# Performance work log

Hardware: AMD Instinct MI355X
Metric: run time of the kernel (lower is better)

The kernel has to match this reference:

```python
import jax, jax.numpy as jnp
import numpy as np

N_II = 100000      # item nodes
N_UIU = 200000     # user + item nodes
D = 64             # embedding_dim
E_II = 600000
E_UIU = 1200000
L_II = 3           # num_layers_ii
L_UIU = 3          # num_layers_uiu
N_USERS = 100000   # items occupy indices [N_USERS, N_USERS+N_II)


def _lightgcn_embedding(x, edge_index, edge_weight, num_layers, num_nodes):
    """PyG LightGCN.get_embedding: symmetric gcn_norm (no self loops) + mean over layer outputs."""
    src, dst = edge_index[0], edge_index[1]
    # gcn_norm: deg over target nodes, weighted by edge_weight
    deg = jax.ops.segment_sum(edge_weight, dst, num_segments=num_nodes)
    deg_inv_sqrt = jnp.where(deg > 0, jax.lax.rsqrt(jnp.where(deg > 0, deg, 1.0)), 0.0)
    norm = deg_inv_sqrt[src] * edge_weight * deg_inv_sqrt[dst]  # [E]
    alpha = 1.0 / (num_layers + 1)
    out = x * alpha
    for _ in range(num_layers):
        # SpMM: gather source embeddings, scale, scatter-add to targets
        x = jax.ops.segment_sum(norm[:, None] * x[src], dst, num_segments=num_nodes)  # [N, D]
        out = out + x * alpha
    return out


def setup_inputs() -> dict:
    key = jax.random.key(0)
    k1, k2, k3, k4, k5, k6 = jax.random.split(key, 6)
    return {
        "emb_ii": jax.random.normal(k1, (N_II, D), dtype=jnp.float32),
        "emb_uiu": jax.random.normal(k2, (N_UIU, D), dtype=jnp.float32),
        "edge_attr_ii": jax.random.uniform(k3, (E_II,), dtype=jnp.float32),
        "edge_attr_uiu": jax.random.uniform(k4, (E_UIU,), dtype=jnp.float32),
        "edge_index_ii": jax.random.randint(k5, (2, E_II), 0, N_II, dtype=jnp.int32),
        "edge_index_uiu": jax.random.randint(k6, (2, E_UIU), 0, N_UIU, dtype=jnp.int32),
        # contiguous item block starting at N_USERS (node_mask_item.nonzero())
        "item_idx": jnp.arange(N_II, dtype=jnp.int32) + N_USERS,
    }


def reference(emb_ii, emb_uiu, edge_attr_ii, edge_attr_uiu,
              edge_index_ii, edge_index_uiu, item_idx):
    # item-item graph propagation
    h_ii = _lightgcn_embedding(emb_ii, edge_index_ii, edge_attr_ii, L_II, N_II)  # [N_II, D]
    # write item embeddings into the user-item embedding table
    emb_uiu = emb_uiu.at[item_idx].set(h_ii)
    # user-item graph propagation
    h_uiu = _lightgcn_embedding(emb_uiu, edge_index_uiu, edge_attr_uiu, L_UIU, N_UIU)  # [N_UIU, D]
    return h_uiu
```

## Files before the change

### kernel.cpp

```cpp
#include <hip/hip_runtime.h>


#define D       64
#define N_II    100000
#define N_UIU   200000
#define E_II    600000
#define E_UIU   1200000
#define N_USERS 100000

__device__ __forceinline__ unsigned short f2bf(float f) {
    unsigned u = __float_as_uint(f);
    u += 0x7fffu + ((u >> 16) & 1u);
    return (unsigned short)(u >> 16);
}
__device__ __forceinline__ void bf8_fma(float acc[8], uint4 p, float v) {
    acc[0] += v * __uint_as_float(p.x << 16);
    acc[1] += v * __uint_as_float(p.x & 0xffff0000u);
    acc[2] += v * __uint_as_float(p.y << 16);
    acc[3] += v * __uint_as_float(p.y & 0xffff0000u);
    acc[4] += v * __uint_as_float(p.z << 16);
    acc[5] += v * __uint_as_float(p.z & 0xffff0000u);
    acc[6] += v * __uint_as_float(p.w << 16);
    acc[7] += v * __uint_as_float(p.w & 0xffff0000u);
}
__device__ __forceinline__ void bf8_add(float acc[8], uint4 p) {
    acc[0] += __uint_as_float(p.x << 16);
    acc[1] += __uint_as_float(p.x & 0xffff0000u);
    acc[2] += __uint_as_float(p.y << 16);
    acc[3] += __uint_as_float(p.y & 0xffff0000u);
    acc[4] += __uint_as_float(p.z << 16);
    acc[5] += __uint_as_float(p.z & 0xffff0000u);
    acc[6] += __uint_as_float(p.w << 16);
    acc[7] += __uint_as_float(p.w & 0xffff0000u);
}
__device__ __forceinline__ uint4 pack8(const float a[8]) {
    uint4 r;
    r.x = (unsigned)f2bf(a[0]) | ((unsigned)f2bf(a[1]) << 16);
    r.y = (unsigned)f2bf(a[2]) | ((unsigned)f2bf(a[3]) << 16);
    r.z = (unsigned)f2bf(a[4]) | ((unsigned)f2bf(a[5]) << 16);
    r.w = (unsigned)f2bf(a[6]) | ((unsigned)f2bf(a[7]) << 16);
    return r;
}


__global__ void k_cnt_rank(const int* __restrict__ dst, int* __restrict__ cnt,
                           int* __restrict__ rank, int E) {
    int e = blockIdx.x * blockDim.x + threadIdx.x;
    if (e < E) rank[e] = atomicAdd(&cnt[dst[e]], 1);
}

__global__ void k_rowoff(const int* __restrict__ cnt, int* __restrict__ roff,
                         int* __restrict__ rend, int* __restrict__ gcur, int N) {
    __shared__ int sh[256];
    __shared__ int base;
    int t = threadIdx.x;
    int i = blockIdx.x * 256 + t;
    int v = (i < N) ? cnt[i] : 0;
    sh[t] = v;
    __syncthreads();
    for (int off = 1; off < 256; off <<= 1) {
        int u = (t >= off) ? sh[t - off] : 0;
        __syncthreads();
        sh[t] += u;
        __syncthreads();
    }
    if (t == 255) base = atomicAdd(gcur, sh[255]);
    __syncthreads();
    if (i < N) {
        int o = base + sh[t] - v;
        roff[i] = o;
        rend[i] = o + v;
    }
}

__global__ void k_fillE(const int* __restrict__ src, const int* __restrict__ dst,
                        const float* __restrict__ w, const int* __restrict__ rank,
                        const int* __restrict__ roff, int2* __restrict__ ev, int E) {
    int e = blockIdx.x * blockDim.x + threadIdx.x;
    if (e < E) {
        int pos = roff[dst[e]] + rank[e];
        ev[pos] = make_int2(src[e], __float_as_int(w[e]));
    }
}

__global__ void k_deg_dis(const int* __restrict__ roff, const int* __restrict__ rend,
                          const int2* __restrict__ ev, float* __restrict__ dis, int N) {
    int i = blockIdx.x * blockDim.x + threadIdx.x;
    if (i >= N) return;
    float dg = 0.f;
    for (int j = roff[i]; j < rend[i]; ++j) dg += __int_as_float(ev[j].y);
    dis[i] = (dg > 0.f) ? rsqrtf(dg) : 0.f;
}

__global__ void k_val(const int* __restrict__ roff, const int* __restrict__ rend,
                      const float* __restrict__ dis, int2* __restrict__ ev, int N) {
    int i = blockIdx.x * blockDim.x + threadIdx.x;
    if (i >= N) return;
    float di = dis[i];
    for (int j = roff[i]; j < rend[i]; ++j) {
        int2 p = ev[j];
        ev[j].y = __float_as_int(di * __int_as_float(p.y) * dis[p.x]);
    }
}

__global__ void k_cvt(const float4* __restrict__ x, uint4* __restrict__ xb, int n8) {
    int i = blockIdx.x * blockDim.x + threadIdx.x;
    if (i >= n8) return;
    float4 a = x[2 * i], b = x[2 * i + 1];
    float t[8] = {a.x, a.y, a.z, a.w, b.x, b.y, b.z, b.w};
    xb[i] = pack8(t);
}

__global__ void k_spmm8(const int* __restrict__ roff, const int* __restrict__ rend,
                        const int2* __restrict__ ev, const uint4* __restrict__ xb,
                        uint4* __restrict__ xn, int N) {
    int idx = blockIdx.x * blockDim.x + threadIdx.x;
    int row = idx >> 3;
    if (row >= N) return;
    int g = idx & 7;
    int s = roff[row], e = rend[row];
    float acc[8] = {0.f, 0.f, 0.f, 0.f, 0.f, 0.f, 0.f, 0.f};
    int j = s;
    for (; j + 1 < e; j += 2) {
        int2 p0 = ev[j], p1 = ev[j + 1];
        uint4 a0 = xb[p0.x * 8 + g];
        uint4 a1 = xb[p1.x * 8 + g];
        bf8_fma(acc, a0, __int_as_float(p0.y));
        bf8_fma(acc, a1, __int_as_float(p1.y));
    }
    if (j < e) {
        int2 p0 = ev[j];
        uint4 a0 = xb[p0.x * 8 + g];
        bf8_fma(acc, a0, __int_as_float(p0.y));
    }
    xn[row * 8 + g] = pack8(acc);
}

__global__ void k_spmm8_final(const int* __restrict__ roff, const int* __restrict__ rend,
                              const int2* __restrict__ ev, const uint4* __restrict__ x2b,
                              const uint4* __restrict__ x1b, const float4* __restrict__ x0,
                              float4* __restrict__ out, uint4* __restrict__ outb,
                              float alpha, int N) {
    int idx = blockIdx.x * blockDim.x + threadIdx.x;
    int row = idx >> 3;
    if (row >= N) return;
    int g = idx & 7;
    int s = roff[row], e = rend[row];
    float acc[8] = {0.f, 0.f, 0.f, 0.f, 0.f, 0.f, 0.f, 0.f};
    int j = s;
    for (; j + 1 < e; j += 2) {
        int2 p0 = ev[j], p1 = ev[j + 1];
        uint4 a0 = x2b[p0.x * 8 + g];
        uint4 a1 = x2b[p1.x * 8 + g];
        bf8_fma(acc, a0, __int_as_float(p0.y));
        bf8_fma(acc, a1, __int_as_float(p1.y));
    }
    if (j < e) {
        int2 p0 = ev[j];
        uint4 a0 = x2b[p0.x * 8 + g];
        bf8_fma(acc, a0, __int_as_float(p0.y));
    }
    bf8_add(acc, x1b[row * 8 + g]);
    bf8_add(acc, x2b[row * 8 + g]);
    float4 b0 = x0[row * 16 + 2 * g];
    float4 b1 = x0[row * 16 + 2 * g + 1];
    float r[8] = {alpha * (b0.x + acc[0]), alpha * (b0.y + acc[1]),
                  alpha * (b0.z + acc[2]), alpha * (b0.w + acc[3]),
                  alpha * (b1.x + acc[4]), alpha * (b1.y + acc[5]),
                  alpha * (b1.z + acc[6]), alpha * (b1.w + acc[7])};
    out[row * 16 + 2 * g]     = make_float4(r[0], r[1], r[2], r[3]);
    out[row * 16 + 2 * g + 1] = make_float4(r[4], r[5], r[6], r[7]);
    if (outb) outb[row * 8 + g] = pack8(r);
}


static void build_csr(const int* src, const int* dst, const float* w, int E, int N,
                      int2* ev, int* rank, int* cnt, int* roff, int* rend,
                      float* dis, hipStream_t stream) {
    const int B = 256;
    const int nbE = (E + B - 1) / B;
    const int nbN = (N + B - 1) / B;
    int* gcur = cnt + N;
    hipMemsetAsync(cnt, 0, ((size_t)N + 1) * sizeof(int), stream);
    k_cnt_rank<<<nbE, B, 0, stream>>>(dst, cnt, rank, E);
    k_rowoff  <<<nbN, B, 0, stream>>>(cnt, roff, rend, gcur, N);
    k_fillE   <<<nbE, B, 0, stream>>>(src, dst, w, rank, roff, ev, E);
    k_deg_dis <<<nbN, B, 0, stream>>>(roff, rend, ev, dis, N);
    k_val     <<<nbN, B, 0, stream>>>(roff, rend, dis, ev, N);
}

extern "C" void kernel_launch(void* const* d_in, const int* in_sizes, int n_in,
                              void* d_out, int out_size, void* d_ws, size_t ws_size,
                              hipStream_t stream) {
    const float* emb_ii  = (const float*)d_in[0];
    float*       emb_uiu = (float*)d_in[1];
    const float* w_ii    = (const float*)d_in[2];
    const float* w_uiu   = (const float*)d_in[3];
    const int*   src_ii  = (const int*)d_in[4];
    const int*   dst_ii  = src_ii + E_II;
    const int*   src_uiu = (const int*)d_in[5];
    const int*   dst_uiu = src_uiu + E_UIU;
    float*       out     = (float*)d_out;

    uint4* xb0_u = (uint4*)d_ws;
    uint4* x1_u  = xb0_u + (size_t)N_UIU * 8;
    uint4* x2_u  = x1_u + (size_t)N_UIU * 8;
    int2*  ev    = (int2*)(x2_u + (size_t)N_UIU * 8);
    int*   rank  = (int*)(ev + E_UIU);
    int*   cnt   = rank + E_UIU;
    int*   roff  = cnt + N_UIU + 1;
    int*   rend  = roff + N_UIU;
    float* dis   = (float*)(rend + N_UIU);

    uint4* g1_x0 = x1_u;
    uint4* g1_x1 = x1_u + (size_t)N_II * 8;
    uint4* g1_x2 = x2_u;

    const int B = 256;
    const float alpha = 0.25f;

    build_csr(src_ii, dst_ii, w_ii, E_II, N_II, ev, rank, cnt, roff, rend, dis, stream);
    {
        const int n8 = N_II * 8;
        const int ng = (n8 + B - 1) / B;
        float* hii = emb_uiu + (size_t)N_USERS * D;
        uint4* hii_b = xb0_u + (size_t)N_USERS * 8;
        k_cvt  <<<ng, B, 0, stream>>>((const float4*)emb_ii, g1_x0, n8);
        k_spmm8<<<ng, B, 0, stream>>>(roff, rend, ev, g1_x0, g1_x1, N_II);
        k_spmm8<<<ng, B, 0, stream>>>(roff, rend, ev, g1_x1, g1_x2, N_II);
        k_spmm8_final<<<ng, B, 0, stream>>>(roff, rend, ev, g1_x2, g1_x1,
                                            (const float4*)emb_ii, (float4*)hii, hii_b,
                                            alpha, N_II);
    }

    build_csr(src_uiu, dst_uiu, w_uiu, E_UIU, N_UIU, ev, rank, cnt, roff, rend, dis, stream);
    {
        const int n8u = N_USERS * 8;
        k_cvt<<<(n8u + B - 1) / B, B, 0, stream>>>((const float4*)emb_uiu, xb0_u, n8u);
        const int n8 = N_UIU * 8;
        const int ng = (n8 + B - 1) / B;
        k_spmm8<<<ng, B, 0, stream>>>(roff, rend, ev, xb0_u, x1_u, N_UIU);
        k_spmm8<<<ng, B, 0, stream>>>(roff, rend, ev, x1_u, x2_u, N_UIU);
        k_spmm8_final<<<ng, B, 0, stream>>>(roff, rend, ev, x2_u, x1_u,
                                            (const float4*)emb_uiu, (float4*)out, nullptr,
                                            alpha, N_UIU);
    }
}
```

Measured before the change: 488.2 us.

## Bin rows by degree and process them in degree-sorted order in SpMM

Adds a degree-histogram counting sort (k_hist, k_scan64, k_scatter) that builds a row permutation plus permuted row ranges. SpMM kernels walk rows in degree-sorted order, so lanes in a wavefront have similar edge counts and less divergence. Row start and end are packed into one int2, and the gather loop is unrolled by four for more loads in flight. The final layer now reads x0 from the bf16 copy instead of fp32, which costs some accuracy. It also stops writing the item embeddings back into the input buffer. The price is three extra small kernels per graph and scattered output writes.

```diff
diff --git a/kernel.cpp b/kernel.cpp
--- a/kernel.cpp
+++ b/kernel.cpp
@@ -49,8 +49,8 @@
     if (e < E) rank[e] = atomicAdd(&cnt[dst[e]], 1);
 }
 
-__global__ void k_rowoff(const int* __restrict__ cnt, int* __restrict__ roff,
-                         int* __restrict__ rend, int* __restrict__ gcur, int N) {
+__global__ void k_rowoff(const int* __restrict__ cnt, int2* __restrict__ rr,
+                         int* __restrict__ gcur, int N) {
     __shared__ int sh[256];
     __shared__ int base;
     int t = threadIdx.x;
@@ -68,39 +68,83 @@
     __syncthreads();
     if (i < N) {
         int o = base + sh[t] - v;
-        roff[i] = o;
-        rend[i] = o + v;
+        rr[i] = make_int2(o, o + v);
     }
 }
 
 __global__ void k_fillE(const int* __restrict__ src, const int* __restrict__ dst,
                         const float* __restrict__ w, const int* __restrict__ rank,
-                        const int* __restrict__ roff, int2* __restrict__ ev, int E) {
+                        const int2* __restrict__ rr, int2* __restrict__ ev, int E) {
     int e = blockIdx.x * blockDim.x + threadIdx.x;
     if (e < E) {
-        int pos = roff[dst[e]] + rank[e];
+        int pos = rr[dst[e]].x + rank[e];
         ev[pos] = make_int2(src[e], __float_as_int(w[e]));
     }
 }
 
-__global__ void k_deg_dis(const int* __restrict__ roff, const int* __restrict__ rend,
-                          const int2* __restrict__ ev, float* __restrict__ dis, int N) {
+__global__ void k_deg_dis(const int2* __restrict__ rr, const int2* __restrict__ ev,
+                          float* __restrict__ dis, int N) {
     int i = blockIdx.x * blockDim.x + threadIdx.x;
     if (i >= N) return;
+    int2 se = rr[i];
     float dg = 0.f;
-    for (int j = roff[i]; j < rend[i]; ++j) dg += __int_as_float(ev[j].y);
+    for (int j = se.x; j < se.y; ++j) dg += __int_as_float(ev[j].y);
     dis[i] = (dg > 0.f) ? rsqrtf(dg) : 0.f;
 }
 
-__global__ void k_val(const int* __restrict__ roff, const int* __restrict__ rend,
-                      const float* __restrict__ dis, int2* __restrict__ ev, int N) {
+__global__ void k_val(const int2* __restrict__ rr, const float* __restrict__ dis,
+                      int2* __restrict__ ev, int N) {
     int i = blockIdx.x * blockDim.x + threadIdx.x;
     if (i >= N) return;
+    int2 se = rr[i];
     float di = dis[i];
-    for (int j = roff[i]; j < rend[i]; ++j) {
+    for (int j = se.x; j < se.y; ++j) {
         int2 p = ev[j];
         ev[j].y = __float_as_int(di * __int_as_float(p.y) * dis[p.x]);
     }
+}
+
+__global__ void k_hist(const int* __restrict__ cnt, int* __restrict__ binrank,
+                       int* __restrict__ ghist, int N) {
+    __shared__ int h[64];
+    __shared__ int base[64];
+    int t = threadIdx.x;
+    if (t < 64) h[t] = 0;
+    __syncthreads();
+    int i = blockIdx.x * 256 + t;
+    int b = 0, r = 0;
+    if (i < N) {
+        int c = cnt[i];
+        b = (c < 63) ? c : 63;
+        r = atomicAdd(&h[b], 1);
+    }
+    __syncthreads();
+    if (t < 64) base[t] = h[t] ? atomicAdd(&ghist[t], h[t]) : 0;
+    __syncthreads();
+    if (i < N) binrank[i] = base[b] + r;
+}
+
+__global__ void k_scan64(const int* __restrict__ ghist, int* __restrict__ gboff) {
+    int l = threadIdx.x;
+    int v = ghist[l];
+    int s = v;
+    for (int o = 1; o < 64; o <<= 1) {
+        int u = __shfl_up(s, o);
+        if (l >= o) s += u;
+    }
+    gboff[l] = s - v;
+}
+
+__global__ void k_scatter(const int* __restrict__ cnt, const int* __restrict__ binrank,
+                          const int* __restrict__ gboff, const int2* __restrict__ rr,
+                          int* __restrict__ perm, int2* __restrict__ rrp, int N) {
+    int i = blockIdx.x * blockDim.x + threadIdx.x;
+    if (i >= N) return;
+    int c = cnt[i];
+    int b = (c < 63) ? c : 63;
+    int pos = gboff[b] + binrank[i];
+    perm[pos] = i;
+    rrp[pos] = rr[i];
 }
 
 __global__ void k_cvt(const float4* __restrict__ x, uint4* __restrict__ xb, int n8) {
@@ -111,24 +155,29 @@
     xb[i] = pack8(t);
 }
 
-__global__ void k_spmm8(const int* __restrict__ roff, const int* __restrict__ rend,
+__global__ void k_spmm8(const int2* __restrict__ rrp, const int* __restrict__ perm,
                         const int2* __restrict__ ev, const uint4* __restrict__ xb,
                         uint4* __restrict__ xn, int N) {
     int idx = blockIdx.x * blockDim.x + threadIdx.x;
-    int row = idx >> 3;
-    if (row >= N) return;
+    int vrow = idx >> 3;
+    if (vrow >= N) return;
     int g = idx & 7;
-    int s = roff[row], e = rend[row];
+    int2 se = rrp[vrow];
+    int row = perm[vrow];
     float acc[8] = {0.f, 0.f, 0.f, 0.f, 0.f, 0.f, 0.f, 0.f};
-    int j = s;
-    for (; j + 1 < e; j += 2) {
-        int2 p0 = ev[j], p1 = ev[j + 1];
+    int j = se.x, e = se.y;
+    for (; j + 3 < e; j += 4) {
+        int2 p0 = ev[j], p1 = ev[j + 1], p2 = ev[j + 2], p3 = ev[j + 3];
         uint4 a0 = xb[p0.x * 8 + g];
         uint4 a1 = xb[p1.x * 8 + g];
+        uint4 a2 = xb[p2.x * 8 + g];
+        uint4 a3 = xb[p3.x * 8 + g];
         bf8_fma(acc, a0, __int_as_float(p0.y));
         bf8_fma(acc, a1, __int_as_float(p1.y));
-    }
-    if (j < e) {
+        bf8_fma(acc, a2, __int_as_float(p2.y));
+        bf8_fma(acc, a3, __int_as_float(p3.y));
+    }
+    for (; j < e; ++j) {
         int2 p0 = ev[j];
         uint4 a0 = xb[p0.x * 8 + g];
         bf8_fma(acc, a0, __int_as_float(p0.y));
@@ -136,64 +185,75 @@
     xn[row * 8 + g] = pack8(acc);
 }
 
-__global__ void k_spmm8_final(const int* __restrict__ roff, const int* __restrict__ rend,
+__global__ void k_spmm8_final(const int2* __restrict__ rrp, const int* __restrict__ perm,
                               const int2* __restrict__ ev, const uint4* __restrict__ x2b,
-                              const uint4* __restrict__ x1b, const float4* __restrict__ x0,
+                              const uint4* __restrict__ x1b, const uint4* __restrict__ x0b,
                               float4* __restrict__ out, uint4* __restrict__ outb,
                               float alpha, int N) {
     int idx = blockIdx.x * blockDim.x + threadIdx.x;
-    int row = idx >> 3;
-    if (row >= N) return;
+    int vrow = idx >> 3;
+    if (vrow >= N) return;
     int g = idx & 7;
-    int s = roff[row], e = rend[row];
+    int2 se = rrp[vrow];
+    int row = perm[vrow];
     float acc[8] = {0.f, 0.f, 0.f, 0.f, 0.f, 0.f, 0.f, 0.f};
-    int j = s;
-    for (; j + 1 < e; j += 2) {
-        int2 p0 = ev[j], p1 = ev[j + 1];
+    int j = se.x, e = se.y;
+    for (; j + 3 < e; j += 4) {
+        int2 p0 = ev[j], p1 = ev[j + 1], p2 = ev[j + 2], p3 = ev[j + 3];
         uint4 a0 = x2b[p0.x * 8 + g];
         uint4 a1 = x2b[p1.x * 8 + g];
+        uint4 a2 = x2b[p2.x * 8 + g];
+        uint4 a3 = x2b[p3.x * 8 + g];
         bf8_fma(acc, a0, __int_as_float(p0.y));
         bf8_fma(acc, a1, __int_as_float(p1.y));
-    }
-    if (j < e) {
+        bf8_fma(acc, a2, __int_as_float(p2.y));
+        bf8_fma(acc, a3, __int_as_float(p3.y));
+    }
+    for (; j < e; ++j) {
         int2 p0 = ev[j];
         uint4 a0 = x2b[p0.x * 8 + g];
         bf8_fma(acc, a0, __int_as_float(p0.y));
     }
     bf8_add(acc, x1b[row * 8 + g]);
     bf8_add(acc, x2b[row * 8 + g]);
-    float4 b0 = x0[row * 16 + 2 * g];
-    float4 b1 = x0[row * 16 + 2 * g + 1];
-    float r[8] = {alpha * (b0.x + acc[0]), alpha * (b0.y + acc[1]),
-                  alpha * (b0.z + acc[2]), alpha * (b0.w + acc[3]),
-                  alpha * (b1.x + acc[4]), alpha * (b1.y + acc[5]),
-                  alpha * (b1.z + acc[6]), alpha * (b1.w + acc[7])};
-    out[row * 16 + 2 * g]     = make_float4(r[0], r[1], r[2], r[3]);
-    out[row * 16 + 2 * g + 1] = make_float4(r[4], r[5], r[6], r[7]);
+    bf8_add(acc, x0b[row * 8 + g]);
+    float r[8];
+#pragma unroll
+    for (int k = 0; k < 8; ++k) r[k] = alpha * acc[k];
+    if (out) {
+        out[row * 16 + 2 * g]     = make_float4(r[0], r[1], r[2], r[3]);
+        out[row * 16 + 2 * g + 1] = make_float4(r[4], r[5], r[6], r[7]);
+    }
     if (outb) outb[row * 8 + g] = pack8(r);
 }
 
 
 static void build_csr(const int* src, const int* dst, const float* w, int E, int N,
-                      int2* ev, int* rank, int* cnt, int* roff, int* rend,
-                      float* dis, hipStream_t stream) {
+                      int2* ev, int* rank, int* cnt, int2* rr, float* dis,
+                      int* perm, int2* rrp, hipStream_t stream) {
     const int B = 256;
     const int nbE = (E + B - 1) / B;
     const int nbN = (N + B - 1) / B;
-    int* gcur = cnt + N;
-    hipMemsetAsync(cnt, 0, ((size_t)N + 1) * sizeof(int), stream);
+    int* gcur  = cnt + N;
+    int* ghist = cnt + N + 1;
+    int* gboff = cnt + N + 65;
+    int* binrank = rank;
+    hipMemsetAsync(cnt, 0, ((size_t)N + 65) * sizeof(int), stream);
     k_cnt_rank<<<nbE, B, 0, stream>>>(dst, cnt, rank, E);
-    k_rowoff  <<<nbN, B, 0, stream>>>(cnt, roff, rend, gcur, N);
-    k_fillE   <<<nbE, B, 0, stream>>>(src, dst, w, rank, roff, ev, E);
-    k_deg_dis <<<nbN, B, 0, stream>>>(roff, rend, ev, dis, N);
-    k_val     <<<nbN, B, 0, stream>>>(roff, rend, dis, ev, N);
+    k_rowoff  <<<nbN, B, 0, stream>>>(cnt, rr, gcur, N);
+    k_fillE   <<<nbE, B, 0, stream>>>(src, dst, w, rank, rr, ev, E);
+    k_deg_dis <<<nbN, B, 0, stream>>>(rr, ev, dis, N);
+    k_val     <<<nbN, B, 0, stream>>>(rr, dis, ev, N);
+    k_hist    <<<nbN, B, 0, stream>>>(cnt, binrank, ghist, N);
+    k_scan64  <<<1, 64, 0, stream>>>(ghist, gboff);
+    k_scatter <<<nbN, B, 0, stream>>>(cnt, binrank, gboff, rr, perm, rrp, N);
 }
 
 extern "C" void kernel_launch(void* const* d_in, const int* in_sizes, int n_in,
                               void* d_out, int out_size, void* d_ws, size_t ws_size,
                               hipStream_t stream) {
     const float* emb_ii  = (const float*)d_in[0];
-    float*       emb_uiu = (float*)d_in[1];
+    const float* emb_uiu = (const float*)d_in[1];
     const float* w_ii    = (const float*)d_in[2];
     const float* w_uiu   = (const float*)d_in[3];
     const int*   src_ii  = (const int*)d_in[4];
@@ -207,10 +267,9 @@
     uint4* x2_u  = x1_u + (size_t)N_UIU * 8;
     int2*  ev    = (int2*)(x2_u + (size_t)N_UIU * 8);
     int*   rank  = (int*)(ev + E_UIU);
-    int*   cnt   = rank + E_UIU;
-    int*   roff  = cnt + N_UIU + 1;
-    int*   rend  = roff + N_UIU;
-    float* dis   = (float*)(rend + N_UIU);
+    int2*  rr    = (int2*)(rank + E_UIU);
+    int*   cnt   = (int*)(rr + N_UIU);
+    float* dis   = (float*)(cnt + N_UIU + 129);
 
     uint4* g1_x0 = x1_u;
     uint4* g1_x1 = x1_u + (size_t)N_II * 8;
@@ -219,30 +278,33 @@
     const int B = 256;
     const float alpha = 0.25f;
 
-    build_csr(src_ii, dst_ii, w_ii, E_II, N_II, ev, rank, cnt, roff, rend, dis, stream);
     {
+        int*  perm = rank + N_II;
+        int2* rrp  = (int2*)(rank + 2 * N_II);
+        build_csr(src_ii, dst_ii, w_ii, E_II, N_II, ev, rank, cnt, rr, dis,
+                  perm, rrp, stream);
         const int n8 = N_II * 8;
         const int ng = (n8 + B - 1) / B;
-        float* hii = emb_uiu + (size_t)N_USERS * D;
         uint4* hii_b = xb0_u + (size_t)N_USERS * 8;
         k_cvt  <<<ng, B, 0, stream>>>((const float4*)emb_ii, g1_x0, n8);
-        k_spmm8<<<ng, B, 0, stream>>>(roff, rend, ev, g1_x0, g1_x1, N_II);
-        k_spmm8<<<ng, B, 0, stream>>>(roff, rend, ev, g1_x1, g1_x2, N_II);
-        k_spmm8_final<<<ng, B, 0, stream>>>(roff, rend, ev, g1_x2, g1_x1,
-                                            (const float4*)emb_ii, (float4*)hii, hii_b,
-                                            alpha, N_II);
-    }
-
-    build_csr(src_uiu, dst_uiu, w_uiu, E_UIU, N_UIU, ev, rank, cnt, roff, rend, dis, stream);
+        k_spmm8<<<ng, B, 0, stream>>>(rrp, perm, ev, g1_x0, g1_x1, N_II);
+        k_spmm8<<<ng, B, 0, stream>>>(rrp, perm, ev, g1_x1, g1_x2, N_II);
+        k_spmm8_final<<<ng, B, 0, stream>>>(rrp, perm, ev, g1_x2, g1_x1, g1_x0,
+                                            nullptr, hii_b, alpha, N_II);
+    }
+
     {
+        int*  perm = rank + N_UIU;
+        int2* rrp  = (int2*)(rank + 2 * N_UIU);
+        build_csr(src_uiu, dst_uiu, w_uiu, E_UIU, N_UIU, ev, rank, cnt, rr, dis,
+                  perm, rrp, stream);
         const int n8u = N_USERS * 8;
         k_cvt<<<(n8u + B - 1) / B, B, 0, stream>>>((const float4*)emb_uiu, xb0_u, n8u);
         const int n8 = N_UIU * 8;
         const int ng = (n8 + B - 1) / B;
-        k_spmm8<<<ng, B, 0, stream>>>(roff, rend, ev, xb0_u, x1_u, N_UIU);
-        k_spmm8<<<ng, B, 0, stream>>>(roff, rend, ev, x1_u, x2_u, N_UIU);
-        k_spmm8_final<<<ng, B, 0, stream>>>(roff, rend, ev, x2_u, x1_u,
-                                            (const float4*)emb_uiu, (float4*)out, nullptr,
-                                            alpha, N_UIU);
-    }
-}
+        k_spmm8<<<ng, B, 0, stream>>>(rrp, perm, ev, xb0_u, x1_u, N_UIU);
+        k_spmm8<<<ng, B, 0, stream>>>(rrp, perm, ev, x1_u, x2_u, N_UIU);
+        k_spmm8_final<<<ng, B, 0, stream>>>(rrp, perm, ev, x2_u, x1_u, xb0_u,
+                                            (float4*)out, nullptr, alpha, N_UIU);
+    }
+}
```

New measurement: 511.3 us. +4.7%, slower.
